# Optimization experiments

Hardware: AMD Instinct MI355X
Metric: run time of the kernel (lower is better)

The kernel has to match this reference:

```python
import jax, jax.numpy as jnp
import numpy as np

NUM_ITERATIONS = 3


def squash(s):
    # s: [..., out_channels]; norm over last axis (matches torch squash on squeezed tensor)
    norm = jnp.linalg.norm(s, axis=-1, keepdims=True)
    return (norm ** 2 / (1.0 + norm ** 2)) * (s / norm)


def setup_inputs() -> dict:
    key = jax.random.key(0)
    k1, k2 = jax.random.split(key)
    B, R, C, O, I = 256, 192, 96, 16, 20
    x = jax.random.normal(k1, (B, R, I), dtype=jnp.float32)
    W = jax.random.normal(k2, (R, C, O, I), dtype=jnp.float32)
    return {"x": x, "W": W}


def reference(x, W):
    # u_hat[b,r,c,o] = W[r,c,o,i] @ x[b,r,i]  (torch: matmul(W, x[i]) per batch element)
    u_hat = jnp.einsum('rcoi,bri->brco', W, x)  # [B,R,C,O]
    R, C = W.shape[0], W.shape[1]
    b_ij = jnp.zeros((R, C), dtype=x.dtype)  # shared across batch (torch b_ij is [1,R,C,1])
    v_j = None
    for it in range(NUM_ITERATIONS):
        c_ij = jax.nn.softmax(b_ij, axis=0)                 # softmax over routes (dim=1 in torch)
        s_j = jnp.einsum('rc,brco->bco', c_ij, u_hat)        # weighted sum over routes
        v_j = squash(s_j)                                    # [B,C,O]
        if it < NUM_ITERATIONS - 1:
            # agreement: <u_hat, v_j> averaged over batch (torch mean(dim=0))
            a_ij = jnp.einsum('brco,bco->rc', u_hat, v_j) / x.shape[0]
            b_ij = b_ij + a_ij
    return v_j  # [B, num_capsules, out_channels] (torch returns trailing singleton [B,C,O,1])
```

## Files before the change

kernel.cpp:

```cpp
#include <hip/hip_runtime.h>


#define R_ 192
#define C_ 96
#define O_ 16
#define I_ 20
#define B_ 256
#define K1 3840
#define N_ 1536
#define ZSPLIT 20
#define STILE 393216

typedef unsigned short u16;
typedef __attribute__((ext_vector_type(8))) short short8;
typedef __attribute__((ext_vector_type(4))) float floatx4;

__device__ inline float bf2f(u16 h) {
  union { unsigned int u; float f; } x; x.u = ((unsigned int)h) << 16; return x.f;
}
__device__ inline u16 f2bf(float f) {
  union { float f; unsigned int u; } x; x.f = f;
  unsigned int r = x.u + 0x7FFFu + ((x.u >> 16) & 1u);
  return (u16)(r >> 16);
}
__device__ inline unsigned int pack2(float a, float b) {
  return (unsigned int)f2bf(a) | ((unsigned int)f2bf(b) << 16);
}
__device__ inline void async16(const u16* g, u16* l) {
  __builtin_amdgcn_global_load_lds(
      (__attribute__((address_space(1))) void*)(unsigned long long)g,
      (__attribute__((address_space(3))) void*)(unsigned int)(unsigned long long)l,
      16, 0, 0);
}

__global__ void k_prep(const float* __restrict__ W, const float* __restrict__ X,
                       u16* __restrict__ WtT, u16* __restrict__ Xk,
                       u16* __restrict__ xT, float* __restrict__ bij) {
  int bid = blockIdx.x;
  if (bid < 5760) {
    int t = (bid * 256 + threadIdx.x) << 2;
    int n = t / K1, k = t - n * K1;
    int c = n >> 4, o = n & 15;
    const float* Wn = W + (size_t)(c * O_ + o) * I_;
    u16 h[4];
    #pragma unroll
    for (int e = 0; e < 4; ++e) {
      int ke = k + e, r = ke / I_, i = ke - r * I_;
      h[e] = f2bf(Wn[(size_t)r * (C_ * O_ * I_) + i]);
    }
    ushort4 o4; o4.x = h[0]; o4.y = h[1]; o4.z = h[2]; o4.w = h[3];
    *(ushort4*)&WtT[t] = o4;
  } else if (bid < 6000) {
    __shared__ u16 tile[64][72];
    int idx = bid - 5760;
    int kb = (idx % 60) << 6, bb = (idx / 60) << 6;
    int brow = threadIdx.x >> 4;
    int kq = (threadIdx.x & 15) << 2;
    #pragma unroll
    for (int p = 0; p < 4; ++p) {
      int bl = p * 16 + brow;
      float4 v = *(const float4*)(X + (size_t)(bb + bl) * K1 + kb + kq);
      ushort4 h;
      h.x = f2bf(v.x); h.y = f2bf(v.y); h.z = f2bf(v.z); h.w = f2bf(v.w);
      *(ushort4*)(Xk + (size_t)(bb + bl) * K1 + kb + kq) = h;
      tile[kq + 0][bl] = h.x;
      tile[kq + 1][bl] = h.y;
      tile[kq + 2][bl] = h.z;
      tile[kq + 3][bl] = h.w;
    }
    __syncthreads();
    int kr = threadIdx.x >> 3;
    int bq = (threadIdx.x & 7) << 3;
    #pragma unroll
    for (int q = 0; q < 2; ++q) {
      int kl = q * 32 + kr;
      *(uint4*)(xT + (size_t)(kb + kl) * B_ + bb + bq) = *(const uint4*)&tile[kl][bq];
    }
  } else {
    int t = ((bid - 6000) * 256 + threadIdx.x) << 2;
    if (t < R_ * C_) *(float4*)&bij[t] = (float4){0.f, 0.f, 0.f, 0.f};
  }
}

__device__ inline uint4 scale_b8(uint4 raw, int kg, const float* smrow) {
  int r0 = kg / I_;
  int bnd = (r0 + 1) * I_ - kg;
  float s0 = smrow[r0];
  float s1 = smrow[(r0 + 1 < R_) ? r0 + 1 : R_ - 1];
  union { uint4 q; u16 h[8]; } u; u.q = raw;
  #pragma unroll
  for (int j = 0; j < 8; ++j)
    u.h[j] = f2bf(bf2f(u.h[j]) * ((j < bnd) ? s0 : s1));
  return u.q;
}

__global__ __launch_bounds__(256) void gemm1(
    const u16* __restrict__ A, const u16* __restrict__ Bt,
    const float* __restrict__ bij, u16* __restrict__ P) {
  __shared__ u16 As[2][128 * 32];
  __shared__ u16 Bs[2][128 * 32];
  __shared__ float sm[8][192];
  int tid = threadIdx.x;
  {
    int cg = tid >> 5, lr = tid & 31;
    int c = (blockIdx.y << 3) + cg;
    float e[6]; float mx = -1e30f;
    #pragma unroll
    for (int j = 0; j < 6; ++j) {
      e[j] = bij[c * R_ + lr + (j << 5)];
      mx = fmaxf(mx, e[j]);
    }
    #pragma unroll
    for (int off = 16; off > 0; off >>= 1) mx = fmaxf(mx, __shfl_xor(mx, off));
    float sum = 0.f;
    #pragma unroll
    for (int j = 0; j < 6; ++j) { e[j] = expf(e[j] - mx); sum += e[j]; }
    #pragma unroll
    for (int off = 16; off > 0; off >>= 1) sum += __shfl_xor(sum, off);
    float inv = 1.0f / sum;
    #pragma unroll
    for (int j = 0; j < 6; ++j) sm[cg][lr + (j << 5)] = e[j] * inv;
  }

  long m0 = (long)blockIdx.x * 128, n0 = (long)blockIdx.y * 128;
  int k0 = blockIdx.z * 192;
  const u16* Ab = A + m0 * K1 + k0;
  const u16* Bb = Bt + n0 * K1 + k0;
  int srow = tid >> 2;
  int scol = (tid & 3) << 3;
  int w = tid >> 6, lane = tid & 63;
  int wm = (w >> 1) << 6, wn = (w & 1) << 6;
  int quad = lane >> 4, lrow = lane & 15;
  int cl0 = srow >> 4;
  int wb = w << 9;
  const u16* Ag0 = Ab + (long)srow * K1 + scol;
  const u16* Ag1 = Ab + (long)(srow + 64) * K1 + scol;
  floatx4 acc[4][4];
  #pragma unroll
  for (int a = 0; a < 4; ++a)
    #pragma unroll
    for (int b = 0; b < 4; ++b) acc[a][b] = (floatx4){0.f, 0.f, 0.f, 0.f};

  async16(Ag0, &As[0][wb]);
  async16(Ag1, &As[0][2048 + wb]);
  uint4 b0 = *(const uint4*)(Bb + (long)srow * K1 + scol);
  uint4 b1 = *(const uint4*)(Bb + (long)(srow + 64) * K1 + scol);
  __syncthreads();

  int p = 0;
  for (int kt = 0; kt < 6; ++kt) {
    int kg = k0 + (kt << 5) + scol;
    ((uint4*)Bs[p])[tid] = scale_b8(b0, kg, &sm[cl0][0]);
    ((uint4*)Bs[p])[tid + 256] = scale_b8(b1, kg, &sm[cl0 + 4][0]);
    __syncthreads();
    if (kt + 1 < 6) {
      int kk = (kt + 1) << 5;
      async16(Ag0 + kk, &As[p ^ 1][wb]);
      async16(Ag1 + kk, &As[p ^ 1][2048 + wb]);
      b0 = *(const uint4*)(Bb + (long)srow * K1 + kk + scol);
      b1 = *(const uint4*)(Bb + (long)(srow + 64) * K1 + kk + scol);
    }
    short8 af[4], bfr[4];
    #pragma unroll
    for (int ms = 0; ms < 4; ++ms)
      af[ms] = *(const short8*)&As[p][(wm + ms * 16 + lrow) * 32 + (quad << 3)];
    #pragma unroll
    for (int ns = 0; ns < 4; ++ns)
      bfr[ns] = *(const short8*)&Bs[p][(wn + ns * 16 + lrow) * 32 + (quad << 3)];
    #pragma unroll
    for (int ms = 0; ms < 4; ++ms)
      #pragma unroll
      for (int ns = 0; ns < 4; ++ns)
        acc[ms][ns] = __builtin_amdgcn_mfma_f32_16x16x32_bf16(
            af[ms], bfr[ns], acc[ms][ns], 0, 0, 0);
    p ^= 1;
  }
  size_t zb = (size_t)blockIdx.z * (size_t)STILE;
  #pragma unroll
  for (int ms = 0; ms < 4; ++ms)
    #pragma unroll
    for (int ns = 0; ns < 4; ++ns) {
      int b = (int)m0 + wm + ms * 16 + (quad << 2);
      int n = (int)n0 + wn + ns * 16 + lrow;
      uint2 pk;
      pk.x = pack2(acc[ms][ns][0], acc[ms][ns][1]);
      pk.y = pack2(acc[ms][ns][2], acc[ms][ns][3]);
      *(uint2*)&P[zb + (size_t)n * B_ + b] = pk;
    }
}

__global__ void k_redsq(const u16* __restrict__ P, float* __restrict__ out,
                        u16* __restrict__ vT, int last) {
  __shared__ float nsq_l[4][128];
  int c = blockIdx.x, bh = blockIdx.y;
  int lane = threadIdx.x & 63, og = threadIdx.x >> 6;
  int bi = (lane << 1);
  int b = (bh << 7) + bi;
  float acc[4][2];
  #pragma unroll
  for (int oo = 0; oo < 4; ++oo) { acc[oo][0] = 0.f; acc[oo][1] = 0.f; }
  for (int z = 0; z < ZSPLIT; ++z) {
    size_t base = (size_t)z * STILE + (size_t)((c << 4) + (og << 2)) * B_ + b;
    #pragma unroll
    for (int oo = 0; oo < 4; ++oo) {
      unsigned int u = *(const unsigned int*)&P[base + (size_t)oo * B_];
      acc[oo][0] += bf2f((u16)(u & 0xffff));
      acc[oo][1] += bf2f((u16)(u >> 16));
    }
  }
  float q0 = 0.f, q1 = 0.f;
  #pragma unroll
  for (int oo = 0; oo < 4; ++oo) {
    q0 += acc[oo][0] * acc[oo][0];
    q1 += acc[oo][1] * acc[oo][1];
  }
  nsq_l[og][bi] = q0;
  nsq_l[og][bi + 1] = q1;
  __syncthreads();
  float n0 = nsq_l[0][bi] + nsq_l[1][bi] + nsq_l[2][bi] + nsq_l[3][bi];
  float n1 = nsq_l[0][bi + 1] + nsq_l[1][bi + 1] + nsq_l[2][bi + 1] + nsq_l[3][bi + 1];
  float f0 = n0 / ((1.0f + n0) * sqrtf(n0));
  float f1 = n1 / ((1.0f + n1) * sqrtf(n1));
  #pragma unroll
  for (int oo = 0; oo < 4; ++oo) { acc[oo][0] *= f0; acc[oo][1] *= f1; }
  if (last) {
    float4 v0 = (float4){acc[0][0], acc[1][0], acc[2][0], acc[3][0]};
    float4 v1 = (float4){acc[0][1], acc[1][1], acc[2][1], acc[3][1]};
    *(float4*)(out + (size_t)b * N_ + (c << 4) + (og << 2)) = v0;
    *(float4*)(out + (size_t)(b + 1) * N_ + (c << 4) + (og << 2)) = v1;
  } else {
    #pragma unroll
    for (int oo = 0; oo < 4; ++oo)
      *(unsigned int*)&vT[(size_t)((c << 4) + (og << 2) + oo) * B_ + b] =
          pack2(acc[oo][0], acc[oo][1]);
  }
}

__global__ __launch_bounds__(256) void gemm2_agree(
    const u16* __restrict__ A, const u16* __restrict__ Bt,
    const u16* __restrict__ WtT, float* __restrict__ bij) {
  const int K = 256;
  __shared__ u16 As[2][128 * 32];
  __shared__ u16 Bs[2][128 * 32];
  int tid = threadIdx.x;
  long m0 = (long)blockIdx.x * 128, n0 = (long)blockIdx.y * 128;
  int k0 = blockIdx.z << 7;
  const u16* Ab = A + m0 * K + k0;
  const u16* Bb = Bt + n0 * K + k0;
  int srow = tid >> 2;
  int scol = (tid & 3) << 3;
  int w = tid >> 6, lane = tid & 63;
  int wm = (w >> 1) << 6, wn = (w & 1) << 6;
  int quad = lane >> 4, lrow = lane & 15;
  int wb = w << 9;
  const u16* Ag0 = Ab + (long)srow * K + scol;
  const u16* Ag1 = Ab + (long)(srow + 64) * K + scol;
  const u16* Bg0 = Bb + (long)srow * K + scol;
  const u16* Bg1 = Bb + (long)(srow + 64) * K + scol;
  floatx4 acc[4][4];
  #pragma unroll
  for (int a = 0; a < 4; ++a)
    #pragma unroll
    for (int b = 0; b < 4; ++b) acc[a][b] = (floatx4){0.f, 0.f, 0.f, 0.f};

  async16(Ag0, &As[0][wb]);
  async16(Ag1, &As[0][2048 + wb]);
  async16(Bg0, &Bs[0][wb]);
  async16(Bg1, &Bs[0][2048 + wb]);

  int p = 0;
  #pragma unroll
  for (int kt = 0; kt < 4; ++kt) {
    __syncthreads();
    if (kt + 1 < 4) {
      int kk = (kt + 1) << 5;
      async16(Ag0 + kk, &As[p ^ 1][wb]);
      async16(Ag1 + kk, &As[p ^ 1][2048 + wb]);
      async16(Bg0 + kk, &Bs[p ^ 1][wb]);
      async16(Bg1 + kk, &Bs[p ^ 1][2048 + wb]);
    }
    short8 af[4], bfr[4];
    #pragma unroll
    for (int ms = 0; ms < 4; ++ms)
      af[ms] = *(const short8*)&As[p][(wm + ms * 16 + lrow) * 32 + (quad << 3)];
    #pragma unroll
    for (int ns = 0; ns < 4; ++ns)
      bfr[ns] = *(const short8*)&Bs[p][(wn + ns * 16 + lrow) * 32 + (quad << 3)];
    #pragma unroll
    for (int ms = 0; ms < 4; ++ms)
      #pragma unroll
      for (int ns = 0; ns < 4; ++ns)
        acc[ms][ns] = __builtin_amdgcn_mfma_f32_16x16x32_bf16(
            af[ms], bfr[ns], acc[ms][ns], 0, 0, 0);
    p ^= 1;
  }
  #pragma unroll
  for (int ms = 0; ms < 4; ++ms) {
    int rowbase = (int)m0 + wm + ms * 16;
    int r_lo = rowbase / I_;
    int r_hi = (rowbase + 15) / I_;
    int bnd = (r_lo + 1) * I_;
    int rowl = rowbase + (quad << 2);
    #pragma unroll
    for (int ns = 0; ns < 4; ++ns) {
      int col = (int)n0 + wn + ns * 16 + lrow;
      uint2 wv = *(const uint2*)&WtT[(size_t)col * K1 + rowl];
      u16 h[4];
      h[0] = (u16)(wv.x & 0xffff); h[1] = (u16)(wv.x >> 16);
      h[2] = (u16)(wv.y & 0xffff); h[3] = (u16)(wv.y >> 16);
      float p0 = 0.f, p1 = 0.f;
      #pragma unroll
      for (int e = 0; e < 4; ++e) {
        float pr = acc[ms][ns][e] * bf2f(h[e]);
        if (rowl + e < bnd) p0 += pr; else p1 += pr;
      }
      #pragma unroll
      for (int off = 32; off > 0; off >>= 1) {
        p0 += __shfl_xor(p0, off);
        p1 += __shfl_xor(p1, off);
      }
      if (lane == 0) {
        int c = col >> 4;
        atomicAdd(&bij[c * R_ + r_lo], p0 * (1.0f / 256.0f));
        atomicAdd(&bij[c * R_ + r_hi], p1 * (1.0f / 256.0f));
      }
    }
  }
}

extern "C" void kernel_launch(void* const* d_in, const int* in_sizes, int n_in,
                              void* d_out, int out_size, void* d_ws, size_t ws_size,
                              hipStream_t stream) {
  const float* X = (const float*)d_in[0];
  const float* W = (const float*)d_in[1];
  float* out = (float*)d_out;
  char* ws = (char*)d_ws;
  u16*  WtT = (u16*)(ws);
  u16*  Xk  = (u16*)(ws + 11796480);
  u16*  xT  = (u16*)(ws + 13762560);
  u16*  vT  = (u16*)(ws + 15728640);
  u16*  Pb  = (u16*)(ws + 16515072);
  float* bij = (float*)(ws + 32243712);

  k_prep<<<6018, 256, 0, stream>>>(W, X, WtT, Xk, xT, bij);

  for (int it = 0; it < 3; ++it) {
    gemm1<<<dim3(2, 12, ZSPLIT), 256, 0, stream>>>(Xk, WtT, bij, Pb);
    k_redsq<<<dim3(96, 2), 256, 0, stream>>>(Pb, out, vT, it == 2);
    if (it < 2)
      gemm2_agree<<<dim3(30, 12, 2), 256, 0, stream>>>(xT, vT, WtT, bij);
  }
}
```

Measured before the change: 167.5 us.

## Skip softmax scaling on first iteration, widen reduce grid, drop gemm2 K-split

The first routing iteration has uniform softmax weights of 1/192, so gemm1 skips the per-element softmax scaling of B there and k_redsq applies 1/192 after the sum. k_redsq now has each thread handle one batch element instead of two, doubling its grid for more parallelism. gemm2_agree no longer splits K across two z-blocks and loops over the full K in each block, which halves its launched blocks and likely removes split-K atomic accumulation into bij. The unscaled first pass changes bf16 rounding slightly, and the single-z gemm2 exposes less parallelism.

```diff
diff --git a/kernel.cpp b/kernel.cpp
--- a/kernel.cpp
+++ b/kernel.cpp
@@ -96,12 +96,12 @@
 
 __global__ __launch_bounds__(256) void gemm1(
     const u16* __restrict__ A, const u16* __restrict__ Bt,
-    const float* __restrict__ bij, u16* __restrict__ P) {
+    const float* __restrict__ bij, u16* __restrict__ P, int doScale) {
   __shared__ u16 As[2][128 * 32];
   __shared__ u16 Bs[2][128 * 32];
   __shared__ float sm[8][192];
   int tid = threadIdx.x;
-  {
+  if (doScale) {
     int cg = tid >> 5, lr = tid & 31;
     int c = (blockIdx.y << 3) + cg;
     float e[6]; float mx = -1e30f;
@@ -149,9 +149,14 @@
 
   int p = 0;
   for (int kt = 0; kt < 6; ++kt) {
-    int kg = k0 + (kt << 5) + scol;
-    ((uint4*)Bs[p])[tid] = scale_b8(b0, kg, &sm[cl0][0]);
-    ((uint4*)Bs[p])[tid + 256] = scale_b8(b1, kg, &sm[cl0 + 4][0]);
+    if (doScale) {
+      int kg = k0 + (kt << 5) + scol;
+      ((uint4*)Bs[p])[tid] = scale_b8(b0, kg, &sm[cl0][0]);
+      ((uint4*)Bs[p])[tid + 256] = scale_b8(b1, kg, &sm[cl0 + 4][0]);
+    } else {
+      ((uint4*)Bs[p])[tid] = b0;
+      ((uint4*)Bs[p])[tid + 256] = b1;
+    }
     __syncthreads();
     if (kt + 1 < 6) {
       int kk = (kt + 1) << 5;
@@ -190,49 +195,37 @@
 }
 
 __global__ void k_redsq(const u16* __restrict__ P, float* __restrict__ out,
-                        u16* __restrict__ vT, int last) {
-  __shared__ float nsq_l[4][128];
+                        u16* __restrict__ vT, float preScale, int last) {
+  __shared__ float nsq_l[4][64];
   int c = blockIdx.x, bh = blockIdx.y;
   int lane = threadIdx.x & 63, og = threadIdx.x >> 6;
-  int bi = (lane << 1);
-  int b = (bh << 7) + bi;
-  float acc[4][2];
-  #pragma unroll
-  for (int oo = 0; oo < 4; ++oo) { acc[oo][0] = 0.f; acc[oo][1] = 0.f; }
+  int b = (bh << 6) + lane;
+  int n0 = (c << 4) + (og << 2);
+  float acc[4];
+  #pragma unroll
+  for (int oo = 0; oo < 4; ++oo) acc[oo] = 0.f;
+  #pragma unroll
   for (int z = 0; z < ZSPLIT; ++z) {
-    size_t base = (size_t)z * STILE + (size_t)((c << 4) + (og << 2)) * B_ + b;
-    #pragma unroll
-    for (int oo = 0; oo < 4; ++oo) {
-      unsigned int u = *(const unsigned int*)&P[base + (size_t)oo * B_];
-      acc[oo][0] += bf2f((u16)(u & 0xffff));
-      acc[oo][1] += bf2f((u16)(u >> 16));
-    }
-  }
-  float q0 = 0.f, q1 = 0.f;
-  #pragma unroll
-  for (int oo = 0; oo < 4; ++oo) {
-    q0 += acc[oo][0] * acc[oo][0];
-    q1 += acc[oo][1] * acc[oo][1];
-  }
-  nsq_l[og][bi] = q0;
-  nsq_l[og][bi + 1] = q1;
+    size_t base = (size_t)z * STILE + (size_t)n0 * B_ + b;
+    #pragma unroll
+    for (int oo = 0; oo < 4; ++oo)
+      acc[oo] += bf2f(P[base + (size_t)oo * B_]);
+  }
+  #pragma unroll
+  for (int oo = 0; oo < 4; ++oo) acc[oo] *= preScale;
+  float q = acc[0] * acc[0] + acc[1] * acc[1] + acc[2] * acc[2] + acc[3] * acc[3];
+  nsq_l[og][lane] = q;
   __syncthreads();
-  float n0 = nsq_l[0][bi] + nsq_l[1][bi] + nsq_l[2][bi] + nsq_l[3][bi];
-  float n1 = nsq_l[0][bi + 1] + nsq_l[1][bi + 1] + nsq_l[2][bi + 1] + nsq_l[3][bi + 1];
-  float f0 = n0 / ((1.0f + n0) * sqrtf(n0));
-  float f1 = n1 / ((1.0f + n1) * sqrtf(n1));
-  #pragma unroll
-  for (int oo = 0; oo < 4; ++oo) { acc[oo][0] *= f0; acc[oo][1] *= f1; }
+  float nsq = nsq_l[0][lane] + nsq_l[1][lane] + nsq_l[2][lane] + nsq_l[3][lane];
+  float f = nsq / ((1.0f + nsq) * sqrtf(nsq));
+  #pragma unroll
+  for (int oo = 0; oo < 4; ++oo) acc[oo] *= f;
   if (last) {
-    float4 v0 = (float4){acc[0][0], acc[1][0], acc[2][0], acc[3][0]};
-    float4 v1 = (float4){acc[0][1], acc[1][1], acc[2][1], acc[3][1]};
-    *(float4*)(out + (size_t)b * N_ + (c << 4) + (og << 2)) = v0;
-    *(float4*)(out + (size_t)(b + 1) * N_ + (c << 4) + (og << 2)) = v1;
+    *(float4*)(out + (size_t)b * N_ + n0) = (float4){acc[0], acc[1], acc[2], acc[3]};
   } else {
     #pragma unroll
     for (int oo = 0; oo < 4; ++oo)
-      *(unsigned int*)&vT[(size_t)((c << 4) + (og << 2) + oo) * B_ + b] =
-          pack2(acc[oo][0], acc[oo][1]);
+      vT[(size_t)(n0 + oo) * B_ + b] = f2bf(acc[oo]);
   }
 }
 
@@ -244,9 +237,8 @@
   __shared__ u16 Bs[2][128 * 32];
   int tid = threadIdx.x;
   long m0 = (long)blockIdx.x * 128, n0 = (long)blockIdx.y * 128;
-  int k0 = blockIdx.z << 7;
-  const u16* Ab = A + m0 * K + k0;
-  const u16* Bb = Bt + n0 * K + k0;
+  const u16* Ab = A + m0 * K;
+  const u16* Bb = Bt + n0 * K;
   int srow = tid >> 2;
   int scol = (tid & 3) << 3;
   int w = tid >> 6, lane = tid & 63;
@@ -270,9 +262,9 @@
 
   int p = 0;
   #pragma unroll
-  for (int kt = 0; kt < 4; ++kt) {
+  for (int kt = 0; kt < 8; ++kt) {
     __syncthreads();
-    if (kt + 1 < 4) {
+    if (kt + 1 < 8) {
       int kk = (kt + 1) << 5;
       async16(Ag0 + kk, &As[p ^ 1][wb]);
       async16(Ag1 + kk, &As[p ^ 1][2048 + wb]);
@@ -345,9 +337,10 @@
   k_prep<<<6018, 256, 0, stream>>>(W, X, WtT, Xk, xT, bij);
 
   for (int it = 0; it < 3; ++it) {
-    gemm1<<<dim3(2, 12, ZSPLIT), 256, 0, stream>>>(Xk, WtT, bij, Pb);
-    k_redsq<<<dim3(96, 2), 256, 0, stream>>>(Pb, out, vT, it == 2);
+    gemm1<<<dim3(2, 12, ZSPLIT), 256, 0, stream>>>(Xk, WtT, bij, Pb, it > 0);
+    k_redsq<<<dim3(96, 4), 256, 0, stream>>>(
+        Pb, out, vT, it == 0 ? (1.0f / 192.0f) : 1.0f, it == 2);
     if (it < 2)
-      gemm2_agree<<<dim3(30, 12, 2), 256, 0, stream>>>(xT, vT, WtT, bij);
-  }
-}
+      gemm2_agree<<<dim3(30, 12), 256, 0, stream>>>(xT, vT, WtT, bij);
+  }
+}
```

Result: no change. 164.7 us (-1.7%).
